# Kernel tuning notes

Hardware: AMD Instinct MI355X
Metric: run time of the kernel (lower is better)

Reference implementation:

```python
import jax, jax.numpy as jnp
import numpy as np

N_EMBD = 1024
N_HEADS = 16
HEAD_SIZE = N_EMBD // N_HEADS  # 64
B, T = 4, 4096


def setup_inputs() -> dict:
    key = jax.random.key(0)
    kx, kq, kk, kv = jax.random.split(key, 4)
    scale = 1.0 / np.sqrt(N_EMBD)
    x = jax.random.normal(kx, (B, T, N_EMBD), dtype=jnp.float32)
    # torch Linear weight shape: (out_features, in_features)
    Wq = jax.random.normal(kq, (HEAD_SIZE, N_EMBD), dtype=jnp.float32) * scale
    Wk = jax.random.normal(kk, (HEAD_SIZE, N_EMBD), dtype=jnp.float32) * scale
    Wv = jax.random.normal(kv, (HEAD_SIZE, N_EMBD), dtype=jnp.float32) * scale
    return {"x": x, "Wq": Wq, "Wk": Wk, "Wv": Wv}


def reference(x, Wq, Wk, Wv):
    # q,k,v: [B, T, H]  (H = head_size)
    q = jnp.einsum('btc,hc->bth', x, Wq)
    k = jnp.einsum('btc,hc->bth', x, Wk)
    v = jnp.einsum('btc,hc->bth', x, Wv)
    # scores: [B, T, T], scaled by head_size**-0.5
    wei = jnp.einsum('bth,bsh->bts', q, k) * (HEAD_SIZE ** -0.5)
    Tlen = x.shape[1]
    causal = jnp.tril(jnp.ones((Tlen, Tlen), dtype=bool))
    wei = jnp.where(causal, wei, -jnp.inf)
    wei = jax.nn.softmax(wei, axis=-1)
    # dropout p=0.0 (eval) -> identity
    out = jnp.einsum('bts,bsh->bth', wei, v)  # [B, T, H]
    return out
```

## Files before the change

kernel.cpp:

```cpp
#include <hip/hip_runtime.h>
#include <math.h>

#define B_ 4
#define T_ 4096
#define C_ 1024
#define H_ 64
#define NROW (B_ * T_)

typedef unsigned short u16;
typedef __attribute__((ext_vector_type(8))) short short8;
typedef __attribute__((ext_vector_type(4))) float floatx4;
typedef __attribute__((ext_vector_type(8))) unsigned short ushortx8;
typedef __attribute__((ext_vector_type(4))) unsigned short ushortx4;

__device__ __forceinline__ u16 f2bf(float f) {
  unsigned int u = __builtin_bit_cast(unsigned int, f);
  unsigned int r = (u + 0x7FFFu + ((u >> 16) & 1u)) >> 16;
  return (u16)r;
}

__global__ __launch_bounds__(256) void cast_w_kernel(
    const float* __restrict__ Wq, const float* __restrict__ Wk,
    const float* __restrict__ Wv, u16* __restrict__ Wb) {
  int i = blockIdx.x * 256 + threadIdx.x;
  const float* src = (i < 16384) ? Wq : ((i < 32768) ? Wk : Wv);
  int j = i & 16383;
  float4 v = ((const float4*)src)[j];
  ushortx4 o = {f2bf(v.x), f2bf(v.y), f2bf(v.z), f2bf(v.w)};
  *(ushortx4*)(Wb + (size_t)i * 4) = o;
}

__global__ __launch_bounds__(256) void proj9_kernel(
    const float* __restrict__ x, const u16* __restrict__ Wb,
    u16* __restrict__ Qb, u16* __restrict__ Kb, u16* __restrict__ Vt) {
  const int m0 = (int)blockIdx.x * 64;
  const int tid = threadIdx.x;
  const int wave = tid >> 6, lane = tid & 63;
  const int lq = lane & 15, quad = lane >> 4;

  __shared__ __align__(16) u16 xs[64 * 1024];

  const u16* wp0 = Wb + (size_t)((wave * 3 + 0) * 16 + lq) * C_ + quad * 8;
  const u16* wp1 = Wb + (size_t)((wave * 3 + 1) * 16 + lq) * C_ + quad * 8;
  const u16* wp2 = Wb + (size_t)((wave * 3 + 2) * 16 + lq) * C_ + quad * 8;
  short8 wf[4][3];
#pragma unroll
  for (int d = 0; d < 4; ++d) {
    wf[d][0] = *(const short8*)(wp0 + d * 32);
    wf[d][1] = *(const short8*)(wp1 + d * 32);
    wf[d][2] = *(const short8*)(wp2 + d * 32);
  }

#pragma unroll 4
  for (int i = 0; i < 32; ++i) {
    int g = i * 256 + tid;
    int row = g >> 7, c = g & 127;
    const float* src = x + (size_t)(m0 + row) * C_ + c * 8;
    float4 a = *(const float4*)(src);
    float4 b = *(const float4*)(src + 4);
    ushortx8 v = {f2bf(a.x), f2bf(a.y), f2bf(a.z), f2bf(a.w),
                  f2bf(b.x), f2bf(b.y), f2bf(b.z), f2bf(b.w)};
    *(ushortx8*)&xs[(row * 128 + (c ^ (row & 7))) * 8] = v;
  }
  __syncthreads();

  floatx4 acc[4][3];
#pragma unroll
  for (int rt = 0; rt < 4; ++rt)
#pragma unroll
    for (int j = 0; j < 3; ++j) acc[rt][j] = (floatx4){0.f, 0.f, 0.f, 0.f};

#pragma unroll
  for (int s = 0; s < 32; ++s) {
    short8 af[4];
#pragma unroll
    for (int rt = 0; rt < 4; ++rt) {
      int row = rt * 16 + lq;
      int c = (s * 4 + quad) ^ (lq & 7);
      af[rt] = *(const short8*)&xs[(row * 128 + c) * 8];
    }
    const int sl = s & 3;
#pragma unroll
    for (int j = 0; j < 3; ++j) {
      short8 bf = wf[sl][j];
#pragma unroll
      for (int rt = 0; rt < 4; ++rt)
        acc[rt][j] =
            __builtin_amdgcn_mfma_f32_16x16x32_bf16(af[rt], bf, acc[rt][j], 0, 0, 0);
    }
    if (s + 4 < 32) {
      wf[sl][0] = *(const short8*)(wp0 + (s + 4) * 32);
      wf[sl][1] = *(const short8*)(wp1 + (s + 4) * 32);
      wf[sl][2] = *(const short8*)(wp2 + (s + 4) * 32);
    }
  }

  __syncthreads();
  u16(*sm)[208] = (u16(*)[208])xs;
#pragma unroll
  for (int j = 0; j < 3; ++j) {
    const int gc = (wave * 3 + j) * 16;
    const float sc = (gc < 64) ? 0.18033688011112042f : 1.0f;
#pragma unroll
    for (int rt = 0; rt < 4; ++rt)
#pragma unroll
      for (int r = 0; r < 4; ++r)
        sm[rt * 16 + quad * 4 + r][gc + lq] = f2bf(acc[rt][j][r] * sc);
  }
  __syncthreads();

  const int row = tid >> 2, hseg = (tid & 3) * 16;
  {
    ushortx8 w0 = *(const ushortx8*)&sm[row][hseg];
    ushortx8 w1 = *(const ushortx8*)&sm[row][hseg + 8];
    u16* dq = Qb + (size_t)(m0 + row) * H_ + hseg;
    *(ushortx8*)dq = w0;
    *(ushortx8*)(dq + 8) = w1;
  }
  {
    ushortx8 w0 = *(const ushortx8*)&sm[row][64 + hseg];
    ushortx8 w1 = *(const ushortx8*)&sm[row][64 + hseg + 8];
    u16* dk = Kb + (size_t)(m0 + row) * H_ + hseg;
    *(ushortx8*)dk = w0;
    *(ushortx8*)(dk + 8) = w1;
  }
  {
    const int h = tid >> 2, tseg = (tid & 3) * 16;
    u16 tmp[16];
#pragma unroll
    for (int tt = 0; tt < 16; ++tt) tmp[tt] = sm[tseg + tt][128 + h];
    ushortx8 w0, w1;
#pragma unroll
    for (int tt = 0; tt < 8; ++tt) { w0[tt] = tmp[tt]; w1[tt] = tmp[8 + tt]; }
    const int bb = m0 >> 12, t0 = m0 & 4095;
    u16* dv = Vt + ((size_t)bb * H_ + h) * T_ + t0 + tseg;
    *(ushortx8*)dv = w0;
    *(ushortx8*)(dv + 8) = w1;
  }
}

__global__ __launch_bounds__(256) void attn_kernel(
    const u16* __restrict__ Qb, const u16* __restrict__ Kb,
    const u16* __restrict__ Vt, float* __restrict__ Opart,
    float* __restrict__ lpart, int KS, int kslog) {
  const int tau = (int)gridDim.x - 1 - (int)blockIdx.x;
  const int q0 = tau * 128;
  const int b = (int)blockIdx.y >> kslog;
  const int s = (int)blockIdx.y & (KS - 1);
  const int tid = threadIdx.x;
  const int wave = tid >> 6, lane = tid & 63;
  const int lq = lane & 15, quad = lane >> 4;
  const int sw = lq & 7;

  __shared__ __align__(16) u16 ksh[2][64 * 64];
  __shared__ __align__(16) u16 vsh[2][64 * 64];
  __shared__ __align__(16) u16 ps[4][32 * 72];

  const int nch = 2 * tau + 2;
  const u16* Kb_b = Kb + (size_t)b * T_ * H_;
  const u16* Vt_b = Vt + (size_t)b * H_ * T_;

  short8 qa[2][2];
#pragma unroll
  for (int rt = 0; rt < 2; ++rt) {
    const u16* qrow =
        Qb + ((size_t)b * T_ + q0 + wave * 32 + rt * 16 + lq) * H_;
    qa[rt][0] = *(const short8*)(qrow + quad * 8);
    qa[rt][1] = *(const short8*)(qrow + 32 + quad * 8);
  }

  floatx4 o[2][4];
  float lrow[2] = {0.f, 0.f};
#pragma unroll
  for (int rt = 0; rt < 2; ++rt)
#pragma unroll
    for (int t = 0; t < 4; ++t) o[rt][t] = (floatx4){0.f, 0.f, 0.f, 0.f};

  const float nbias = -5.770780163555852f;

  const int srow = tid >> 3;
  const int sseg = tid & 7;
  const int spos0 = (srow * 8 + (sseg ^ (srow & 7))) * 8;
  const int spos1 = spos0 + 2048;

  int4 kst0, kst1, vst0, vst1;
#define STAGE_LOAD(S0)                                                        \
  {                                                                           \
    kst0 = *(const int4*)(Kb_b + (size_t)((S0) + srow) * H_ + sseg * 8);      \
    kst1 = *(const int4*)(Kb_b + (size_t)((S0) + srow + 32) * H_ + sseg * 8); \
    vst0 = *(const int4*)(Vt_b + (size_t)srow * T_ + (S0) + sseg * 8);        \
    vst1 = *(const int4*)(Vt_b + (size_t)(srow + 32) * T_ + (S0) + sseg * 8); \
  }
#define STAGE_WRITE(BUF)                                                      \
  {                                                                           \
    *(int4*)&ksh[BUF][spos0] = kst0;                                          \
    *(int4*)&ksh[BUF][spos1] = kst1;                                          \
    *(int4*)&vsh[BUF][spos0] = vst0;                                          \
    *(int4*)&vsh[BUF][spos1] = vst1;                                          \
  }

  int ch = s, buf = 0;
  if (ch < nch) {
    STAGE_LOAD(ch * 64)
    STAGE_WRITE(0)
  }
  __syncthreads();

  if (ch < nch) {
    const int qmaxw = q0 + wave * 32 + 31;
    for (;;) {
      const bool have_next = (ch + KS < nch);
      if (have_next) { STAGE_LOAD((ch + KS) * 64) }
      const int s0 = ch * 64;

      if (s0 <= qmaxw) {
        floatx4 z[2][4];
#pragma unroll
        for (int t = 0; t < 4; ++t) {
          const int row8 = (t * 16 + lq) * 8;
          short8 kb0 = *(const short8*)&ksh[buf][(row8 + (quad ^ sw)) * 8];
          short8 kb1 = *(const short8*)&ksh[buf][(row8 + ((quad + 4) ^ sw)) * 8];
#pragma unroll
          for (int rt = 0; rt < 2; ++rt) {
            floatx4 zz = (floatx4){nbias, nbias, nbias, nbias};
            zz = __builtin_amdgcn_mfma_f32_16x16x32_bf16(kb0, qa[rt][0], zz, 0, 0, 0);
            zz = __builtin_amdgcn_mfma_f32_16x16x32_bf16(kb1, qa[rt][1], zz, 0, 0, 0);
            z[rt][t] = zz;
          }
        }

#pragma unroll
        for (int rt = 0; rt < 2; ++rt) {
          const int qr = q0 + wave * 32 + rt * 16 + lq;
          const bool nm = (s0 + 63 > q0 + wave * 32 + rt * 16);
#pragma unroll
          for (int t = 0; t < 4; ++t) {
            float p0 = exp2f(z[rt][t][0]);
            float p1 = exp2f(z[rt][t][1]);
            float p2 = exp2f(z[rt][t][2]);
            float p3 = exp2f(z[rt][t][3]);
            if (nm) {
              const int k0 = s0 + t * 16 + quad * 4;
              p0 = (k0 + 0 > qr) ? 0.f : p0;
              p1 = (k0 + 1 > qr) ? 0.f : p1;
              p2 = (k0 + 2 > qr) ? 0.f : p2;
              p3 = (k0 + 3 > qr) ? 0.f : p3;
            }
            lrow[rt] += (p0 + p1) + (p2 + p3);
            ushortx4 pk = {f2bf(p0), f2bf(p1), f2bf(p2), f2bf(p3)};
            *(ushortx4*)&ps[wave][(rt * 16 + lq) * 72 + t * 16 + quad * 4] = pk;
          }
        }

        short8 pa[2][2];
#pragma unroll
        for (int rt = 0; rt < 2; ++rt) {
          pa[rt][0] = *(const short8*)&ps[wave][(rt * 16 + lq) * 72 + quad * 8];
          pa[rt][1] =
              *(const short8*)&ps[wave][(rt * 16 + lq) * 72 + 32 + quad * 8];
        }

#pragma unroll
        for (int t = 0; t < 4; ++t) {
          const int row8 = (t * 16 + lq) * 8;
          short8 vb0 = *(const short8*)&vsh[buf][(row8 + (quad ^ sw)) * 8];
          short8 vb1 = *(const short8*)&vsh[buf][(row8 + ((quad + 4) ^ sw)) * 8];
#pragma unroll
          for (int rt = 0; rt < 2; ++rt) {
            o[rt][t] = __builtin_amdgcn_mfma_f32_16x16x32_bf16(pa[rt][0], vb0,
                                                               o[rt][t], 0, 0, 0);
            o[rt][t] = __builtin_amdgcn_mfma_f32_16x16x32_bf16(pa[rt][1], vb1,
                                                               o[rt][t], 0, 0, 0);
          }
        }
      }

      if (!have_next) break;
      STAGE_WRITE(buf ^ 1)
      __syncthreads();
      buf ^= 1;
      ch += KS;
    }
  }

#pragma unroll
  for (int rt = 0; rt < 2; ++rt) {
    lrow[rt] += __shfl_xor(lrow[rt], 16);
    lrow[rt] += __shfl_xor(lrow[rt], 32);
  }

  const size_t prow = (size_t)((b << kslog) + s) * T_ + q0 + wave * 32;
#pragma unroll
  for (int rt = 0; rt < 2; ++rt) {
#pragma unroll
    for (int t = 0; t < 4; ++t)
#pragma unroll
      for (int r = 0; r < 4; ++r)
        Opart[(prow + rt * 16 + quad * 4 + r) * H_ + t * 16 + lq] =
            o[rt][t][r];
    if (quad == 0) lpart[prow + rt * 16 + lq] = lrow[rt];
  }
}

__global__ __launch_bounds__(256) void combine_kernel(
    const float* __restrict__ Opart, const float* __restrict__ lpart,
    float* __restrict__ out, int KS, int kslog) {
  int gid = blockIdx.x * 256 + threadIdx.x;
  int b = gid >> 16;
  int rem = gid & 65535;
  int t = rem >> 4;
  int hs = (rem & 15) * 4;
  float sx = 0.f, sy = 0.f, sz = 0.f, sw = 0.f, ls = 0.f;
  for (int s = 0; s < KS; ++s) {
    size_t row = (size_t)((b << kslog) + s) * T_ + t;
    float4 v = *(const float4*)(Opart + row * H_ + hs);
    sx += v.x; sy += v.y; sz += v.z; sw += v.w;
    ls += lpart[row];
  }
  float inv = 1.f / ls;
  float4 o = make_float4(sx * inv, sy * inv, sz * inv, sw * inv);
  *(float4*)(out + ((size_t)b * T_ + t) * H_ + hs) = o;
}

extern "C" void kernel_launch(void* const* d_in, const int* in_sizes, int n_in,
                              void* d_out, int out_size, void* d_ws, size_t ws_size,
                              hipStream_t stream) {
  const float* x = (const float*)d_in[0];
  const float* Wq = (const float*)d_in[1];
  const float* Wk = (const float*)d_in[2];
  const float* Wv = (const float*)d_in[3];
  u16* Qb = (u16*)d_ws;
  u16* Kb = Qb + (size_t)NROW * H_;
  u16* Vt = Kb + (size_t)NROW * H_;
  u16* Wb = Vt + (size_t)NROW * H_;
  const size_t base = (size_t)3 * NROW * H_ * 2 + 192 * 1024 * 2;

  int KS = 8;
  while (KS > 1 &&
         base + (size_t)KS * ((size_t)B_ * T_ * H_ * 4 + (size_t)B_ * T_ * 4) >
             ws_size)
    KS >>= 1;
  int kslog = (KS == 8) ? 3 : (KS == 4) ? 2 : (KS == 2) ? 1 : 0;

  float* Opart = (float*)((char*)d_ws + base);
  float* lpart = Opart + (size_t)KS * B_ * T_ * H_;
  float* out = (float*)d_out;

  cast_w_kernel<<<dim3(192), 256, 0, stream>>>(Wq, Wk, Wv, Wb);
  proj9_kernel<<<dim3(256), 256, 0, stream>>>(x, Wb, Qb, Kb, Vt);
  attn_kernel<<<dim3(32, B_ * KS), 256, 0, stream>>>(Qb, Kb, Vt, Opart, lpart,
                                                     KS, kslog);
  combine_kernel<<<dim3(1024), 256, 0, stream>>>(Opart, lpart, out, KS, kslog);
}
```

Baseline: 162.6 us.

## Single-buffer K/V shared tiles, raise occupancy hint, use native exp2

Replaces the double-buffered K/V shared-memory tiles with a single buffer, which roughly halves the K/V LDS footprint. The price is a second barrier per chunk so the tile can be overwritten only after all waves finish reading it. It also adds a min-blocks-per-SM launch bound of 4 and swaps exp2f for the hardware exp2 builtin. The aim is more resident blocks to hide latency, at the cost of extra synchronisation and possible register pressure from the launch bound.

```diff
diff --git a/kernel.cpp b/kernel.cpp
--- a/kernel.cpp
+++ b/kernel.cpp
@@ -18,6 +18,12 @@
   unsigned int r = (u + 0x7FFFu + ((u >> 16) & 1u)) >> 16;
   return (u16)r;
 }
+
+#if __has_builtin(__builtin_amdgcn_exp2f)
+#define EXP2(x) __builtin_amdgcn_exp2f(x)
+#else
+#define EXP2(x) __expf((x) * 0.6931471805599453f)
+#endif
 
 __global__ __launch_bounds__(256) void cast_w_kernel(
     const float* __restrict__ Wq, const float* __restrict__ Wk,
@@ -139,7 +145,7 @@
   }
 }
 
-__global__ __launch_bounds__(256) void attn_kernel(
+__global__ __launch_bounds__(256, 4) void attn_kernel(
     const u16* __restrict__ Qb, const u16* __restrict__ Kb,
     const u16* __restrict__ Vt, float* __restrict__ Opart,
     float* __restrict__ lpart, int KS, int kslog) {
@@ -152,8 +158,8 @@
   const int lq = lane & 15, quad = lane >> 4;
   const int sw = lq & 7;
 
-  __shared__ __align__(16) u16 ksh[2][64 * 64];
-  __shared__ __align__(16) u16 vsh[2][64 * 64];
+  __shared__ __align__(16) u16 ksh[64 * 64];
+  __shared__ __align__(16) u16 vsh[64 * 64];
   __shared__ __align__(16) u16 ps[4][32 * 72];
 
   const int nch = 2 * tau + 2;
@@ -191,18 +197,18 @@
     vst0 = *(const int4*)(Vt_b + (size_t)srow * T_ + (S0) + sseg * 8);        \
     vst1 = *(const int4*)(Vt_b + (size_t)(srow + 32) * T_ + (S0) + sseg * 8); \
   }
-#define STAGE_WRITE(BUF)                                                      \
+#define STAGE_WRITE()                                                         \
   {                                                                           \
-    *(int4*)&ksh[BUF][spos0] = kst0;                                          \
-    *(int4*)&ksh[BUF][spos1] = kst1;                                          \
-    *(int4*)&vsh[BUF][spos0] = vst0;                                          \
-    *(int4*)&vsh[BUF][spos1] = vst1;                                          \
-  }
-
-  int ch = s, buf = 0;
+    *(int4*)&ksh[spos0] = kst0;                                               \
+    *(int4*)&ksh[spos1] = kst1;                                               \
+    *(int4*)&vsh[spos0] = vst0;                                               \
+    *(int4*)&vsh[spos1] = vst1;                                               \
+  }
+
+  int ch = s;
   if (ch < nch) {
     STAGE_LOAD(ch * 64)
-    STAGE_WRITE(0)
+    STAGE_WRITE()
   }
   __syncthreads();
 
@@ -218,8 +224,8 @@
 #pragma unroll
         for (int t = 0; t < 4; ++t) {
           const int row8 = (t * 16 + lq) * 8;
-          short8 kb0 = *(const short8*)&ksh[buf][(row8 + (quad ^ sw)) * 8];
-          short8 kb1 = *(const short8*)&ksh[buf][(row8 + ((quad + 4) ^ sw)) * 8];
+          short8 kb0 = *(const short8*)&ksh[(row8 + (quad ^ sw)) * 8];
+          short8 kb1 = *(const short8*)&ksh[(row8 + ((quad + 4) ^ sw)) * 8];
 #pragma unroll
           for (int rt = 0; rt < 2; ++rt) {
             floatx4 zz = (floatx4){nbias, nbias, nbias, nbias};
@@ -235,10 +241,10 @@
           const bool nm = (s0 + 63 > q0 + wave * 32 + rt * 16);
 #pragma unroll
           for (int t = 0; t < 4; ++t) {
-            float p0 = exp2f(z[rt][t][0]);
-            float p1 = exp2f(z[rt][t][1]);
-            float p2 = exp2f(z[rt][t][2]);
-            float p3 = exp2f(z[rt][t][3]);
+            float p0 = EXP2(z[rt][t][0]);
+            float p1 = EXP2(z[rt][t][1]);
+            float p2 = EXP2(z[rt][t][2]);
+            float p3 = EXP2(z[rt][t][3]);
             if (nm) {
               const int k0 = s0 + t * 16 + quad * 4;
               p0 = (k0 + 0 > qr) ? 0.f : p0;
@@ -263,8 +269,8 @@
 #pragma unroll
         for (int t = 0; t < 4; ++t) {
           const int row8 = (t * 16 + lq) * 8;
-          short8 vb0 = *(const short8*)&vsh[buf][(row8 + (quad ^ sw)) * 8];
-          short8 vb1 = *(const short8*)&vsh[buf][(row8 + ((quad + 4) ^ sw)) * 8];
+          short8 vb0 = *(const short8*)&vsh[(row8 + (quad ^ sw)) * 8];
+          short8 vb1 = *(const short8*)&vsh[(row8 + ((quad + 4) ^ sw)) * 8];
 #pragma unroll
           for (int rt = 0; rt < 2; ++rt) {
             o[rt][t] = __builtin_amdgcn_mfma_f32_16x16x32_bf16(pa[rt][0], vb0,
@@ -276,9 +282,9 @@
       }
 
       if (!have_next) break;
-      STAGE_WRITE(buf ^ 1)
       __syncthreads();
-      buf ^= 1;
+      STAGE_WRITE()
+      __syncthreads();
       ch += KS;
     }
   }
```

After: 174.2 us. 7.1% more time.
